# Optimization experiments

Hardware: AMD Instinct MI355X
Metric: run time of the kernel (lower is better)

The kernel has to match this reference:

```python
import jax, jax.numpy as jnp
import numpy as np

# Dims: B nodes, Z species (elements), IN/OUT channels, M = 2*l+1 (l=1)
B, Z, IN, OUT, M = 8192, 10, 512, 512, 3
ALPHA = 1.0 / np.sqrt(IN)  # self.alpha = 1/sqrt(in_dim)
SQRT3 = float(np.sqrt(3.0))


def setup_inputs() -> dict:
    key = jax.random.key(0)
    k1, k2, k3 = jax.random.split(key, 3)
    t = jax.random.normal(k1, (B, IN, M), dtype=jnp.float32)
    species = jax.random.randint(k2, (B,), 0, Z)
    node_attrs = jax.nn.one_hot(species, Z, dtype=jnp.float32)  # [B, Z] one-hot
    # torch.nn.init.uniform_(weights, -sqrt(3), sqrt(3))
    weights = jax.random.uniform(k3, (Z, OUT, IN), dtype=jnp.float32,
                                 minval=-SQRT3, maxval=SQRT3)
    return {"t": t, "node_attrs": node_attrs, "weights": weights}


def reference(t, node_attrs, weights):
    # Faithful to: einsum('bz, zCc, bcd -> bCd', node_attrs, weights*alpha, t)
    # Contract weights with t first per species ([Z,B,C,M], ~500MB), which
    # avoids the huge [B,C,c] per-node weight-gather intermediate, then
    # select/sum over species with the one-hot node_attrs.
    W = weights * ALPHA                       # [Z, OUT, IN]
    zt = jnp.einsum('zCc,bcd->zbCd', W, t)    # [Z, B, OUT, M]
    out = jnp.einsum('bz,zbCd->bCd', node_attrs, zt)  # [B, OUT, M]
    return out
```

## Files before the change

### kernel.cpp

```cpp
#include <hip/hip_runtime.h>
#include <stdint.h>

#define NB   8192
#define NZ   10
#define CIN  512
#define COUT 512
#define MM   3
#define ALPHA 0.04419417382415922f

#define ROWS_TOTAL (NB * MM)
#define BM 128
#define BN 128
#define BK 32
#define KITERS (CIN / BK)
#define MAX_MT (ROWS_TOTAL / BM + NZ)
#define NGRP 32
#define PW_BLOCKS 320
#define PT_BLOCKS 2048

typedef short bf16x8 __attribute__((ext_vector_type(8)));
typedef float f32x4  __attribute__((ext_vector_type(4)));
typedef uint32_t u32x4 __attribute__((ext_vector_type(4)));

__device__ __forceinline__ uint16_t f2bf(float f) {
    union { float f; uint32_t i; } v; v.f = f;
    uint32_t x = v.i;
    x += 0x7fffu + ((x >> 16) & 1u);
    return (uint16_t)(x >> 16);
}
__device__ __forceinline__ uint32_t pack2(float a, float b) {
    return (uint32_t)f2bf(a) | ((uint32_t)f2bf(b) << 16);
}
__device__ __forceinline__ void async16(const ushort* g, ushort* l) {
    __builtin_amdgcn_global_load_lds((const uint32_t*)g, (uint32_t*)l, 16, 0, 0);
}

__global__ __launch_bounds__(256)
void prep_kernel(const float* __restrict__ t, const float* __restrict__ attrs,
                 const float* __restrict__ w, int* __restrict__ species,
                 int* __restrict__ hist, ushort* __restrict__ wt,
                 ushort* __restrict__ tb) {
    const int tid = threadIdx.x;
    const int wv = tid >> 6, lane = tid & 63;

    if (blockIdx.x < NGRP) {
        __shared__ int wc[4][NZ];
        const int b = blockIdx.x * 256 + tid;
        const float* a = attrs + (size_t)b * NZ;
        int s = 0;
        #pragma unroll
        for (int z = 0; z < NZ; z++) if (a[z] > 0.5f) s = z;
        species[b] = s;
        #pragma unroll
        for (int z = 0; z < NZ; z++) {
            unsigned long long m = __ballot(s == z);
            if (lane == 0) wc[wv][z] = __popcll(m);
        }
        __syncthreads();
        if (tid < NZ)
            hist[blockIdx.x * NZ + tid] = wc[0][tid] + wc[1][tid] + wc[2][tid] + wc[3][tid];
    } else if (blockIdx.x < NGRP + PW_BLOCKS) {
        const size_t base = (size_t)(blockIdx.x - NGRP) * 8192;
        #pragma unroll
        for (int e = 0; e < 4; e++) {
            const size_t i = base + ((size_t)e * 256 + tid) * 8;
            f32x4 a = __builtin_nontemporal_load((const f32x4*)(w + i));
            f32x4 b = __builtin_nontemporal_load((const f32x4*)(w + i) + 1);
            u32x4 o;
            o.x = pack2(a.x, a.y); o.y = pack2(a.z, a.w);
            o.z = pack2(b.x, b.y); o.w = pack2(b.z, b.w);
            *(u32x4*)(wt + i) = o;
        }
    } else {
        const int p = (blockIdx.x - NGRP - PW_BLOCKS) * 4 + wv;
        const f32x4* src = (const f32x4*)(t + (size_t)p * (CIN * MM) + lane * 24);
        f32x4 f[6];
        #pragma unroll
        for (int i = 0; i < 6; i++) f[i] = __builtin_nontemporal_load(src + i);
        const float* v = (const float*)f;
        #pragma unroll
        for (int d = 0; d < MM; d++) {
            u32x4 o;
            o.x = pack2(v[d],      v[3 + d]);
            o.y = pack2(v[6 + d],  v[9 + d]);
            o.z = pack2(v[12 + d], v[15 + d]);
            o.w = pack2(v[18 + d], v[21 + d]);
            *(u32x4*)&tb[(size_t)(3 * p + d) * CIN + lane * 8] = o;
        }
    }
}

__global__ __launch_bounds__(256)
void place_kernel(const int* __restrict__ species, const int* __restrict__ hist,
                  int* __restrict__ sorted, int* __restrict__ offsets,
                  int* __restrict__ tile_offsets) {
    __shared__ int lhist[NGRP][NZ];
    __shared__ int loff[NZ + 1], ltoff[NZ + 1];
    __shared__ int pb[NZ];
    __shared__ int wc[4][NZ];
    const int tid = threadIdx.x, g = blockIdx.x;

    for (int i = tid; i < NGRP * NZ; i += 256) ((int*)lhist)[i] = hist[i];
    __syncthreads();
    if (tid == 0) {
        int off = 0, toff = 0;
        for (int z = 0; z < NZ; z++) {
            int tot = 0;
            for (int gg = 0; gg < NGRP; gg++) tot += lhist[gg][z];
            loff[z] = off; ltoff[z] = toff;
            off += tot;
            toff += (3 * tot + BM - 1) / BM;
        }
        loff[NZ] = off; ltoff[NZ] = toff;
    }
    __syncthreads();
    if (tid < NZ) {
        int base = loff[tid];
        for (int gg = 0; gg < g; gg++) base += lhist[gg][tid];
        pb[tid] = base;
    }
    if (g == 0 && tid < NZ + 1) {
        offsets[tid] = loff[tid];
        tile_offsets[tid] = ltoff[tid];
    }
    const int b = g * 256 + tid;
    const int s = species[b];
    const int wv = tid >> 6, lane = tid & 63;
    unsigned long long mymask = 0;
    #pragma unroll
    for (int z = 0; z < NZ; z++) {
        unsigned long long m = __ballot(s == z);
        if (lane == 0) wc[wv][z] = __popcll(m);
        if (s == z) mymask = m;
    }
    __syncthreads();
    int rank = __popcll(mymask & ((1ull << lane) - 1ull));
    #pragma unroll
    for (int w2 = 0; w2 < 4; w2++) if (w2 < wv) rank += wc[w2][s];
    sorted[pb[s] + rank] = b;
}

__global__ __launch_bounds__(256)
void gemm_kernel(const ushort* __restrict__ tb, const ushort* __restrict__ wt,
                 const int* __restrict__ sorted, const int* __restrict__ offsets,
                 const int* __restrict__ tile_offsets, float* __restrict__ out) {
    __shared__ ushort As[BM][BK];
    __shared__ ushort Bs[BN][BK];
    __shared__ int spos[48];

    const int mt = blockIdx.x;
    if (mt >= tile_offsets[NZ]) return;
    int z = 0;
    #pragma unroll
    for (int i = 1; i < NZ; i++) if (tile_offsets[i] <= mt) z = i;

    const int row_base = 3 * offsets[z] + (mt - tile_offsets[z]) * BM;
    const int row_end  = 3 * offsets[z + 1];
    const int pos0     = row_base / 3;
    const int Cbase    = blockIdx.y * BN;

    const int tid = threadIdx.x;
    const int wv = tid >> 6, lane = tid & 63;

    if (tid < 48) spos[tid] = sorted[min(pos0 + tid, NB - 1)];

    const int lrow = lane >> 2;
    const int lk   = (lane & 3) * 8;
    const int r0 = min(row_base + wv * 32 + lrow,      row_end - 1);
    const int r1 = min(row_base + wv * 32 + 16 + lrow, row_end - 1);
    const int p0 = r0 / 3, d0 = r0 - 3 * p0;
    const int p1 = r1 / 3, d1 = r1 - 3 * p1;
    const ushort* gA0 = tb + ((size_t)sorted[p0] * 3 + d0) * CIN + lk;
    const ushort* gA1 = tb + ((size_t)sorted[p1] * 3 + d1) * CIN + lk;
    const ushort* gB0 = wt + ((size_t)z * COUT + Cbase + wv * 32 + lrow) * CIN + lk;
    const ushort* gB1 = gB0 + (size_t)16 * CIN;
    ushort* lA0 = &As[wv * 32][0];
    ushort* lA1 = &As[wv * 32 + 16][0];
    ushort* lB0 = &Bs[wv * 32][0];
    ushort* lB1 = &Bs[wv * 32 + 16][0];

    const int wm = wv & 1, wn = wv >> 1;
    const int q = lane >> 4, mr = lane & 15;

    f32x4 acc[4][4];
    #pragma unroll
    for (int i = 0; i < 4; i++)
        #pragma unroll
        for (int j = 0; j < 4; j++) acc[i][j] = (f32x4){0.f, 0.f, 0.f, 0.f};

    for (int kt = 0; kt < KITERS; kt++) {
        const int ko = kt * BK;
        async16(gA0 + ko, lA0);
        async16(gA1 + ko, lA1);
        async16(gB0 + ko, lB0);
        async16(gB1 + ko, lB1);
        __syncthreads();

        bf16x8 af[4], bf[4];
        #pragma unroll
        for (int am = 0; am < 4; am++)
            af[am] = *(const bf16x8*)&As[wm * 64 + am * 16 + mr][q * 8];
        #pragma unroll
        for (int bn = 0; bn < 4; bn++)
            bf[bn] = *(const bf16x8*)&Bs[wn * 64 + bn * 16 + mr][q * 8];
        #pragma unroll
        for (int am = 0; am < 4; am++)
            #pragma unroll
            for (int bn = 0; bn < 4; bn++)
                acc[am][bn] = __builtin_amdgcn_mfma_f32_16x16x32_bf16(
                    af[am], bf[bn], acc[am][bn], 0, 0, 0);
        __syncthreads();
    }

    #pragma unroll
    for (int am = 0; am < 4; am++) {
        #pragma unroll
        for (int r = 0; r < 4; r++) {
            const int Rg = row_base + wm * 64 + am * 16 + q * 4 + r;
            if (Rg < row_end) {
                const int pos = Rg / 3;
                const int d = Rg - 3 * pos;
                const int node = spos[pos - pos0];
                float* o = out + (size_t)node * (COUT * MM) + d;
                #pragma unroll
                for (int bn = 0; bn < 4; bn++) {
                    const int Cg = Cbase + wn * 64 + bn * 16 + mr;
                    o[(size_t)Cg * 3] = ALPHA * acc[am][bn][r];
                }
            }
        }
    }
}

extern "C" void kernel_launch(void* const* d_in, const int* in_sizes, int n_in,
                              void* d_out, int out_size, void* d_ws, size_t ws_size,
                              hipStream_t stream) {
    const float* t     = (const float*)d_in[0];
    const float* attrs = (const float*)d_in[1];
    const float* w     = (const float*)d_in[2];
    float* out = (float*)d_out;

    uint8_t* ws = (uint8_t*)d_ws;
    int* species      = (int*)ws;                  ws += NB * 4;
    int* sorted       = (int*)ws;                  ws += NB * 4;
    int* hist         = (int*)ws;                  ws += NGRP * NZ * 4;
    int* offsets      = (int*)ws;                  ws += 16 * 4;
    int* tile_offsets = (int*)ws;                  ws += 16 * 4;
    ws = (uint8_t*)(((uintptr_t)ws + 255) & ~(uintptr_t)255);
    ushort* wt = (ushort*)ws;                      ws += (size_t)NZ * COUT * CIN * 2;
    ushort* tb = (ushort*)ws;

    hipLaunchKernelGGL(prep_kernel, dim3(NGRP + PW_BLOCKS + PT_BLOCKS), dim3(256),
                       0, stream, t, attrs, w, species, hist, wt, tb);
    hipLaunchKernelGGL(place_kernel, dim3(NGRP), dim3(256), 0, stream,
                       species, hist, sorted, offsets, tile_offsets);
    hipLaunchKernelGGL(gemm_kernel, dim3(MAX_MT, COUT / BN), dim3(256), 0, stream,
                       tb, wt, sorted, offsets, tile_offsets, out);
}
```

Baseline: 167.2 us.

## Double K tile to 64 with XOR-swizzled LDS and N-major grid order

Raises the GEMM K tile from 32 to 64, which halves the number of K iterations and barrier pairs. Each iteration now issues eight 16-byte async loads per thread and runs two MFMA sub-steps. The LDS column chunks are XOR-swizzled by row to avoid bank conflicts on the wider rows. The grid is transposed so that the four N-blocks of the same row tile launch next to each other, letting them share A rows in cache. The cost is double the LDS footprint per block and more address registers.

Measured after the change: 161.0 us. -3.7%, faster.

```diff
diff --git a/kernel.cpp b/kernel.cpp
--- a/kernel.cpp
+++ b/kernel.cpp
@@ -11,7 +11,7 @@
 #define ROWS_TOTAL (NB * MM)
 #define BM 128
 #define BN 128
-#define BK 32
+#define BK 64
 #define KITERS (CIN / BK)
 #define MAX_MT (ROWS_TOTAL / BM + NZ)
 #define NGRP 32
@@ -148,7 +148,8 @@
     __shared__ ushort Bs[BN][BK];
     __shared__ int spos[48];
 
-    const int mt = blockIdx.x;
+    const int mt = blockIdx.y;
+    const int Cbase = blockIdx.x * BN;
     if (mt >= tile_offsets[NZ]) return;
     int z = 0;
     #pragma unroll
@@ -157,27 +158,22 @@
     const int row_base = 3 * offsets[z] + (mt - tile_offsets[z]) * BM;
     const int row_end  = 3 * offsets[z + 1];
     const int pos0     = row_base / 3;
-    const int Cbase    = blockIdx.y * BN;
 
     const int tid = threadIdx.x;
     const int wv = tid >> 6, lane = tid & 63;
 
     if (tid < 48) spos[tid] = sorted[min(pos0 + tid, NB - 1)];
 
-    const int lrow = lane >> 2;
-    const int lk   = (lane & 3) * 8;
-    const int r0 = min(row_base + wv * 32 + lrow,      row_end - 1);
-    const int r1 = min(row_base + wv * 32 + 16 + lrow, row_end - 1);
-    const int p0 = r0 / 3, d0 = r0 - 3 * p0;
-    const int p1 = r1 / 3, d1 = r1 - 3 * p1;
-    const ushort* gA0 = tb + ((size_t)sorted[p0] * 3 + d0) * CIN + lk;
-    const ushort* gA1 = tb + ((size_t)sorted[p1] * 3 + d1) * CIN + lk;
-    const ushort* gB0 = wt + ((size_t)z * COUT + Cbase + wv * 32 + lrow) * CIN + lk;
-    const ushort* gB1 = gB0 + (size_t)16 * CIN;
-    ushort* lA0 = &As[wv * 32][0];
-    ushort* lA1 = &As[wv * 32 + 16][0];
-    ushort* lB0 = &Bs[wv * 32][0];
-    ushort* lB1 = &Bs[wv * 32 + 16][0];
+    const int sub = lane >> 3;
+    const int kc  = (lane & 7) ^ sub;
+    const ushort* gA[4];
+    #pragma unroll
+    for (int j = 0; j < 4; j++) {
+        const int r = min(row_base + wv * 32 + j * 8 + sub, row_end - 1);
+        const int p = r / 3, d = r - 3 * p;
+        gA[j] = tb + ((size_t)sorted[p] * 3 + d) * CIN + kc * 8;
+    }
+    const ushort* gB = wt + ((size_t)z * COUT + Cbase + wv * 32 + sub) * CIN + kc * 8;
 
     const int wm = wv & 1, wn = wv >> 1;
     const int q = lane >> 4, mr = lane & 15;
@@ -190,25 +186,34 @@
 
     for (int kt = 0; kt < KITERS; kt++) {
         const int ko = kt * BK;
-        async16(gA0 + ko, lA0);
-        async16(gA1 + ko, lA1);
-        async16(gB0 + ko, lB0);
-        async16(gB1 + ko, lB1);
+        #pragma unroll
+        for (int j = 0; j < 4; j++)
+            async16(gA[j] + ko, &As[wv * 32 + j * 8][0]);
+        #pragma unroll
+        for (int j = 0; j < 4; j++)
+            async16(gB + (size_t)(j * 8) * CIN + ko, &Bs[wv * 32 + j * 8][0]);
         __syncthreads();
 
-        bf16x8 af[4], bf[4];
-        #pragma unroll
-        for (int am = 0; am < 4; am++)
-            af[am] = *(const bf16x8*)&As[wm * 64 + am * 16 + mr][q * 8];
-        #pragma unroll
-        for (int bn = 0; bn < 4; bn++)
-            bf[bn] = *(const bf16x8*)&Bs[wn * 64 + bn * 16 + mr][q * 8];
-        #pragma unroll
-        for (int am = 0; am < 4; am++)
+        #pragma unroll
+        for (int s = 0; s < 2; s++) {
+            bf16x8 af[4], bf[4];
             #pragma unroll
-            for (int bn = 0; bn < 4; bn++)
-                acc[am][bn] = __builtin_amdgcn_mfma_f32_16x16x32_bf16(
-                    af[am], bf[bn], acc[am][bn], 0, 0, 0);
+            for (int am = 0; am < 4; am++) {
+                const int ra = wm * 64 + am * 16 + mr;
+                af[am] = *(const bf16x8*)&As[ra][((s * 4 + q) ^ (mr & 7)) * 8];
+            }
+            #pragma unroll
+            for (int bn = 0; bn < 4; bn++) {
+                const int rb = wn * 64 + bn * 16 + mr;
+                bf[bn] = *(const bf16x8*)&Bs[rb][((s * 4 + q) ^ (mr & 7)) * 8];
+            }
+            #pragma unroll
+            for (int am = 0; am < 4; am++)
+                #pragma unroll
+                for (int bn = 0; bn < 4; bn++)
+                    acc[am][bn] = __builtin_amdgcn_mfma_f32_16x16x32_bf16(
+                        af[am], bf[bn], acc[am][bn], 0, 0, 0);
+        }
         __syncthreads();
     }
 
@@ -254,6 +259,6 @@
                        0, stream, t, attrs, w, species, hist, wt, tb);
     hipLaunchKernelGGL(place_kernel, dim3(NGRP), dim3(256), 0, stream,
                        species, hist, sorted, offsets, tile_offsets);
-    hipLaunchKernelGGL(gemm_kernel, dim3(MAX_MT, COUT / BN), dim3(256), 0, stream,
+    hipLaunchKernelGGL(gemm_kernel, dim3(COUT / BN, MAX_MT), dim3(256), 0, stream,
                        tb, wt, sorted, offsets, tile_offsets, out);
 }
```
